# Kernel tuning notes

Measured on AMD Instinct MI355X. Metric: run time of the kernel, lower is better.

## Reference

```python
import jax, jax.numpy as jnp
import numpy as np

H = 16
LN_EPS = 1e-5


def setup_inputs() -> dict:
    key = jax.random.key(0)
    ks = jax.random.split(key, 8)
    B, N, D = 2, 2048, 1024
    s = D ** -0.5
    return {
        "q_s": jax.random.normal(ks[0], (B, N, D), jnp.float32),
        "pos_emb": jax.random.normal(ks[1], (B, N, D), jnp.float32),
        "Wq": jax.random.normal(ks[2], (D, D), jnp.float32) * s,
        "Wk": jax.random.normal(ks[3], (D, D), jnp.float32) * s,
        "Wv": jax.random.normal(ks[4], (D, D), jnp.float32) * s,
        "Wo": jax.random.normal(ks[5], (D, D), jnp.float32) * s,
        "bo": jnp.zeros((D,), jnp.float32),
        "ln_g": jnp.ones((D,), jnp.float32),
        "ln_b": jnp.zeros((D,), jnp.float32),
    }


def _split_heads(t):
    b, n, d = t.shape
    return t.reshape(b, n, H, d // H).transpose(0, 2, 1, 3)  # b h n d


def reference(q_s, pos_emb, Wq, Wk, Wv, Wo, bo, ln_g, ln_b):
    # self-attention: k_s = v_s = q_s
    q = _split_heads(q_s @ Wq)
    k = _split_heads(q_s @ Wk)
    v = _split_heads(q_s @ Wv)
    p = _split_heads(pos_emb)
    scale = q.shape[-1] ** -0.5
    # content-content + content-position attention logits: [b,h,i,j]
    att = (jnp.einsum('bhid,bhjd->bhij', q, k) + jnp.einsum('bhid,bhjd->bhij', q, p)) * scale
    att = jax.nn.softmax(att, axis=-1)
    o = jnp.einsum('bhij,bhjd->bhid', att, v)
    b, h, n, d = o.shape
    o = o.transpose(0, 2, 1, 3).reshape(b, n, h * d)
    o = o @ Wo + bo  # out_layer (dropout rate 0 -> identity)
    x = o + q_s  # residual
    mu = jnp.mean(x, axis=-1, keepdims=True)
    var = jnp.var(x, axis=-1, keepdims=True)
    return (x - mu) * jax.lax.rsqrt(var + LN_EPS) * ln_g + ln_b
```

## Files before the change

kernel.cpp:

```cpp
#include <hip/hip_runtime.h>
#include <hip/hip_bf16.h>
#include <stdint.h>

typedef unsigned short u16;
typedef unsigned int u32;
typedef short s16x8 __attribute__((ext_vector_type(8)));
typedef short s16x4 __attribute__((ext_vector_type(4)));
typedef float f32x4 __attribute__((ext_vector_type(4)));

#define MFMA(a, b, c) __builtin_amdgcn_mfma_f32_16x16x32_bf16((a), (b), (c), 0, 0, 0)

__device__ __forceinline__ float bf2f(u16 h) {
  u32 u = ((u32)h) << 16;
  float f;
  __builtin_memcpy(&f, &u, 4);
  return f;
}

__device__ __forceinline__ u16 f2bf_rte(float f) {
  __hip_bfloat16 h = __float2bfloat16(f);
  u16 u;
  __builtin_memcpy(&u, &h, 2);
  return u;
}

__device__ __forceinline__ void gload16(const u16* g, u16* l) {
  __builtin_amdgcn_global_load_lds((const __attribute__((address_space(1))) u32*)g,
                                   (__attribute__((address_space(3))) u32*)l, 16, 0, 0);
}

__global__ __launch_bounds__(256) void k_prep(const float* __restrict__ q_s,
                                              const float* __restrict__ pos,
                                              const float* __restrict__ W0,
                                              const float* __restrict__ W1,
                                              const float* __restrict__ W2,
                                              const float* __restrict__ W3,
                                              u16* __restrict__ Xbf,
                                              u16* __restrict__ Pp,
                                              u16* __restrict__ WT) {
  __shared__ u16 tile[64][65];
  const int b = blockIdx.x;
  const int t = threadIdx.x;
  if (b < 2048) {
    const int i = b * 256 + t;
    const f32x4* p = (const f32x4*)(q_s + (size_t)i * 8);
    f32x4 a = p[0], bb = p[1];
    s16x8 o;
    for (int k = 0; k < 4; ++k) o[k] = (short)f2bf_rte(a[k]);
    for (int k = 0; k < 4; ++k) o[4 + k] = (short)f2bf_rte(bb[k]);
    *(s16x8*)(Xbf + (size_t)i * 8) = o;
  } else if (b < 3072) {
    const int pb = b - 2048;
    const int bh = pb >> 5, bx = pb & 31;
    const int bq = bh >> 4, h = bh & 15;
    const int n = bx * 64 + (t >> 2);
    const int d0 = (t & 3) * 16;
    const float* src = &pos[((size_t)(bq * 2048 + n)) * 1024 + h * 64 + d0];
    u16* dst = &Pp[((size_t)bh * 2048 + n) * 64 + d0];
    f32x4 a = *(const f32x4*)src;
    f32x4 bq4 = *(const f32x4*)(src + 4);
    f32x4 c = *(const f32x4*)(src + 8);
    f32x4 dq = *(const f32x4*)(src + 12);
    s16x8 o0, o1;
    for (int i = 0; i < 4; ++i) {
      o0[i] = (short)f2bf_rte(a[i]);
      o0[4 + i] = (short)f2bf_rte(bq4[i]);
      o1[i] = (short)f2bf_rte(c[i]);
      o1[4 + i] = (short)f2bf_rte(dq[i]);
    }
    *(s16x8*)dst = o0;
    *(s16x8*)(dst + 8) = o1;
  } else {
    const int wb = b - 3072;
    const int z = wb >> 8, r2 = wb & 255;
    const int bx = r2 & 15, by = r2 >> 4;
    const float* in = (z == 0) ? W0 : (z == 1) ? W1 : (z == 2) ? W2 : W3;
    u16* o = WT + (size_t)z * 1024 * 1024;
    const int tx = t & 63, ty = t >> 6;
    const int r0 = by * 64, c0 = bx * 64;
    for (int rr = 0; rr < 16; ++rr) {
      int row = rr * 4 + ty;
      tile[row][tx] = f2bf_rte(in[(size_t)(r0 + row) * 1024 + c0 + tx]);
    }
    __syncthreads();
    for (int rr = 0; rr < 16; ++rr) {
      int row = rr * 4 + ty;
      o[(size_t)(c0 + row) * 1024 + r0 + tx] = tile[tx][row];
    }
  }
}

__global__ __launch_bounds__(256) void k_transpose_v(const u16* __restrict__ V,
                                                     u16* __restrict__ Vt) {
  __shared__ u16 tile[64][65];
  const int t = threadIdx.x, tx = t & 63, ty = t >> 6;
  const int j0 = blockIdx.x * 64;
  const int bh = blockIdx.y;
  const u16* src = V + (size_t)bh * 2048 * 64;
  u16* dst = Vt + (size_t)bh * 64 * 2048;
  for (int rr = 0; rr < 16; ++rr) {
    int row = rr * 4 + ty;
    tile[row][tx] = src[(size_t)(j0 + row) * 64 + tx];
  }
  __syncthreads();
  for (int rr = 0; rr < 16; ++rr) {
    int d = rr * 4 + ty;
    dst[(size_t)d * 2048 + j0 + tx] = tile[tx][d];
  }
}

__global__ __launch_bounds__(256) void k_qkv_gemm(const u16* __restrict__ X,
                                                  const u16* __restrict__ WT,
                                                  const u16* __restrict__ Pp,
                                                  u16* __restrict__ Qh,
                                                  u16* __restrict__ Kh,
                                                  u16* __restrict__ Vh) {
  __shared__ u16 As[3][4096];
  __shared__ u16 Bs[3][4096];
  const int t = threadIdx.x;
  const int lane = t & 63, wid = t >> 6;
  const int wr = wid >> 1, wc = wid & 1;
  const int g = lane >> 4, lr = lane & 15;
  const int lin = blockIdx.y * 24 + blockIdx.x;
  const int swz = (lin & 7) * 96 + (lin >> 3);
  const int m0 = (swz / 24) * 128, n0 = (swz % 24) * 128;

  const int srcRow = t >> 2;
  const int srcKsw = ((t & 3) * 8) ^ (((t >> 3) & 3) << 3);
  const u16* aSrc = &X[(size_t)(m0 + srcRow) * 1024 + srcKsw];
  const u16* bSrc = &WT[(size_t)(n0 + srcRow) * 1024 + srcKsw];

  const int csw = (g * 8) ^ (((lr >> 1) & 3) << 3);

  f32x4 acc[4][4] = {};

#define QKV_STAGE(buf, k0)                                   \
  {                                                          \
    gload16(aSrc + (k0), &As[buf][wid * 512]);               \
    gload16(aSrc + 65536 + (k0), &As[buf][wid * 512 + 2048]);\
    gload16(bSrc + (k0), &Bs[buf][wid * 512]);               \
    gload16(bSrc + 65536 + (k0), &Bs[buf][wid * 512 + 2048]);\
  }

  QKV_STAGE(0, 0);
  QKV_STAGE(1, 32);
  QKV_STAGE(2, 64);
  for (int k = 0; k < 32; ++k) {
    if (k < 30) {
      asm volatile("s_waitcnt vmcnt(8)" ::: "memory");
    } else if (k == 30) {
      asm volatile("s_waitcnt vmcnt(4)" ::: "memory");
    } else {
      asm volatile("s_waitcnt vmcnt(0)" ::: "memory");
    }
    __builtin_amdgcn_sched_barrier(0);
    __builtin_amdgcn_s_barrier();
    const int cur = k % 3;
    s16x8 a[4], b[4];
#pragma unroll
    for (int mi = 0; mi < 4; ++mi)
      a[mi] = *(const s16x8*)&As[cur][(wr * 64 + mi * 16 + lr) * 32 + csw];
#pragma unroll
    for (int nj = 0; nj < 4; ++nj)
      b[nj] = *(const s16x8*)&Bs[cur][(wc * 64 + nj * 16 + lr) * 32 + csw];
#pragma unroll
    for (int mi = 0; mi < 4; ++mi)
#pragma unroll
      for (int nj = 0; nj < 4; ++nj)
        acc[mi][nj] = MFMA(a[mi], b[nj], acc[mi][nj]);
    __builtin_amdgcn_s_barrier();
    if (k < 29) QKV_STAGE(cur, (k + 3) * 32);
  }
#undef QKV_STAGE

  const float QSCALE = 0.125f * 1.44269504f;
  for (int mi = 0; mi < 4; ++mi) {
    for (int nj = 0; nj < 4; ++nj) {
      const int n_g = n0 + wc * 64 + nj * 16 + lr;
      const int buf = n_g >> 10;
      const int col = n_g & 1023;
      const int h = col >> 6, d = col & 63;
      u16* dst = (buf == 0) ? Qh : ((buf == 1) ? Kh : Vh);
      for (int r = 0; r < 4; ++r) {
        const int row = m0 + wr * 64 + mi * 16 + g * 4 + r;
        const int b = row >> 11, n = row & 2047;
        const size_t off = (size_t)((b * 16 + h) * 2048 + n) * 64 + d;
        float v = acc[mi][nj][r];
        if (buf == 1) v += bf2f(Pp[off]);
        if (buf == 0) v *= QSCALE;
        dst[off] = f2bf_rte(v);
      }
    }
  }
}

__global__ __launch_bounds__(512, 4) void k_attn(const u16* __restrict__ Qh,
                                                 const u16* __restrict__ Kh,
                                                 const u16* __restrict__ Vt,
                                                 u16* __restrict__ Oh) {
  const int t = threadIdx.x, lane = t & 63, wid = t >> 6;
  const int g = lane >> 4, lr = lane & 15;
  const int hid = blockIdx.x;
  const int lid = (hid & 7) * 64 + (hid >> 3);
  const int bh = lid >> 4, itile = lid & 15;
  const int i0 = itile * 128 + wid * 16;

  __shared__ char Ks[4][8192];
  __shared__ char Vs[4][8192];

  const u16* Qp = Qh + (size_t)bh * 2048 * 64;
  const u16* Kp = Kh + (size_t)bh * 2048 * 64;
  const u16* Vp = Vt + (size_t)bh * 64 * 2048;

  s16x8 aq[2];
  aq[0] = *(const s16x8*)&Qp[(size_t)(i0 + lr) * 64 + g * 8];
  aq[1] = *(const s16x8*)&Qp[(size_t)(i0 + lr) * 64 + 32 + g * 8];

  f32x4 oa[4] = {};
  float ms = -1e30f, ls = 0.f;

  const int srow = t >> 3;
  const int sch = (t & 7) * 16;
  const int schS = sch ^ ((srow & 7) << 4);
  const u16* kB = &Kp[(size_t)srow * 64 + (schS >> 1)];
  const u16* vB = &Vp[(size_t)srow * 2048 + (schS >> 1)];

#define ATTN_STAGE(p)                                                \
  {                                                                  \
    gload16(kB + (size_t)(p) * 4096, (u16*)Ks[(p) & 3] + wid * 512); \
    gload16(vB + (size_t)(p) * 64, (u16*)Vs[(p) & 3] + wid * 512);   \
  }

#define ATTN_BODY(BUF)                                                         \
  {                                                                            \
    const char* Kc = Ks[BUF];                                                  \
    const char* Vc = Vs[BUF];                                                  \
    f32x4 s[4] = {};                                                           \
    _Pragma("unroll") for (int jf = 0; jf < 4; ++jf) {                         \
      const int row = jf * 16 + lr;                                            \
      const int bw = (row & 7) << 4;                                           \
      s16x8 bk0 = *(const s16x8*)(Kc + ((row * 128 + g * 16) ^ bw));           \
      s16x8 bk1 = *(const s16x8*)(Kc + ((row * 128 + 64 + g * 16) ^ bw));      \
      s[jf] = MFMA(bk0, aq[0], s[jf]);                                         \
      s[jf] = MFMA(bk1, aq[1], s[jf]);                                         \
    }                                                                          \
    float mj[4];                                                               \
    _Pragma("unroll") for (int jf = 0; jf < 4; ++jf)                           \
        mj[jf] = fmaxf(fmaxf(s[jf][0], s[jf][1]), fmaxf(s[jf][2], s[jf][3]));  \
    float tl = fmaxf(fmaxf(mj[0], mj[1]), fmaxf(mj[2], mj[3]));                \
    if (!__all(tl <= ms + 8.f)) {                                              \
      float tm = fmaxf(tl, __shfl_xor(tl, 16, 64));                            \
      tm = fmaxf(tm, __shfl_xor(tm, 32, 64));                                  \
      float mn = fmaxf(ms, tm);                                                \
      float al = __builtin_amdgcn_exp2f(ms - mn);                              \
      ls *= al;                                                                \
      ms = mn;                                                                 \
      _Pragma("unroll") for (int r = 0; r < 4; ++r) {                          \
        float ab = __shfl(al, g * 4 + r, 64);                                  \
        _Pragma("unroll") for (int df = 0; df < 4; ++df) oa[df][r] *= ab;      \
      }                                                                        \
    }                                                                          \
    float pj[4];                                                               \
    _Pragma("unroll") for (int jf = 0; jf < 4; ++jf) {                         \
      _Pragma("unroll") for (int r = 0; r < 4; ++r)                            \
          s[jf][r] = __builtin_amdgcn_exp2f(s[jf][r] - ms);                    \
      pj[jf] = (s[jf][0] + s[jf][1]) + (s[jf][2] + s[jf][3]);                  \
    }                                                                          \
    ls += (pj[0] + pj[1]) + (pj[2] + pj[3]);                                   \
    u32 pk[4][2];                                                              \
    _Pragma("unroll") for (int jf = 0; jf < 4; ++jf) {                         \
      asm("v_cvt_pk_bf16_f32 %0, %1, %2"                                       \
          : "=v"(pk[jf][0]) : "v"(s[jf][0]), "v"(s[jf][1]));                   \
      asm("v_cvt_pk_bf16_f32 %0, %1, %2"                                       \
          : "=v"(pk[jf][1]) : "v"(s[jf][2]), "v"(s[jf][3]));                   \
    }                                                                          \
    s16x8 pa[2];                                                               \
    _Pragma("unroll") for (int c = 0; c < 2; ++c) {                            \
      u32 w_[4];                                                               \
      _Pragma("unroll") for (int wl = 0; wl < 2; ++wl) {                       \
        u32 A = pk[2 * c][wl], B = pk[2 * c + 1][wl];                          \
        asm("v_permlane32_swap_b32 %0, %1" : "+v"(A), "+v"(B));                \
        asm("v_permlane16_swap_b32 %0, %1" : "+v"(A), "+v"(B));                \
        w_[wl] = A;                                                            \
        w_[2 + wl] = B;                                                        \
      }                                                                        \
      __builtin_memcpy(&pa[c], w_, 16);                                       \
    }                                                                          \
    _Pragma("unroll") for (int df = 0; df < 4; ++df) {                         \
      const int row = df * 16 + lr;                                            \
      const int bw = (row & 7) << 4;                                           \
      s16x8 bv0 = *(const s16x8*)(Vc + ((row * 128 + g * 16) ^ bw));           \
      s16x8 bv1 = *(const s16x8*)(Vc + ((row * 128 + 64 + g * 16) ^ bw));      \
      oa[df] = MFMA(pa[0], bv0, oa[df]);                                       \
      oa[df] = MFMA(pa[1], bv1, oa[df]);                                       \
    }                                                                          \
  }

  ATTN_STAGE(0);
  ATTN_STAGE(1);
  ATTN_STAGE(2);

  for (int tb = 0; tb < 7; ++tb) {
#pragma unroll
    for (int ti = 0; ti < 4; ++ti) {
      const int tt = tb * 4 + ti;
      asm volatile("s_waitcnt vmcnt(4)" ::: "memory");
      __builtin_amdgcn_sched_barrier(0);
      __builtin_amdgcn_s_barrier();
      ATTN_STAGE(tt + 3);
      ATTN_BODY(ti);
    }
  }
  {
    asm volatile("s_waitcnt vmcnt(4)" ::: "memory");
    __builtin_amdgcn_sched_barrier(0);
    __builtin_amdgcn_s_barrier();
    ATTN_STAGE(31);
    ATTN_BODY(0);
  }
  {
    asm volatile("s_waitcnt vmcnt(4)" ::: "memory");
    __builtin_amdgcn_sched_barrier(0);
    __builtin_amdgcn_s_barrier();
    ATTN_BODY(1);
  }
  {
    asm volatile("s_waitcnt vmcnt(2)" ::: "memory");
    __builtin_amdgcn_sched_barrier(0);
    __builtin_amdgcn_s_barrier();
    ATTN_BODY(2);
  }
  {
    asm volatile("s_waitcnt vmcnt(0)" ::: "memory");
    __builtin_amdgcn_sched_barrier(0);
    __builtin_amdgcn_s_barrier();
    ATTN_BODY(3);
  }
#undef ATTN_BODY
#undef ATTN_STAGE

  ls += __shfl_xor(ls, 16, 64);
  ls += __shfl_xor(ls, 32, 64);
  float lb[4];
#pragma unroll
  for (int r = 0; r < 4; ++r) lb[r] = __shfl(ls, g * 4 + r, 64);

  u16* Op = Oh + (size_t)bh * 2048 * 64;
#pragma unroll
  for (int df = 0; df < 4; ++df)
#pragma unroll
    for (int r = 0; r < 4; ++r) {
      const int row0 = i0 + g * 4 + r;
      Op[(size_t)row0 * 64 + df * 16 + lr] = f2bf_rte(oa[df][r] / lb[r]);
    }
}

__global__ __launch_bounds__(256) void k_out_gemm(const u16* __restrict__ Oh,
                                                  const u16* __restrict__ WTo,
                                                  const float* __restrict__ bo,
                                                  const u16* __restrict__ qsb,
                                                  float* __restrict__ X) {
  __shared__ u16 As[3][4096];
  __shared__ u16 Bs[3][4096];
  const int t = threadIdx.x;
  const int lane = t & 63, wid = t >> 6;
  const int wr = wid >> 1, wc = wid & 1;
  const int g = lane >> 4, lr = lane & 15;
  const int lin = blockIdx.y * 8 + blockIdx.x;
  const int swz = (lin & 7) * 32 + (lin >> 3);
  const int m0 = (swz / 8) * 128, n0 = (swz % 8) * 128;

  const int srcRow = t >> 2;
  const int srcKsw = ((t & 3) * 8) ^ (((t >> 3) & 3) << 3);
  const int rg = m0 + srcRow, bb0 = rg >> 11, nn0 = rg & 2047;
  const int rg2 = rg + 64, bb2 = rg2 >> 11, nn2 = rg2 & 2047;
  const u16* bSrc = &WTo[(size_t)(n0 + srcRow) * 1024 + srcKsw];
  const int csw = (g * 8) ^ (((lr >> 1) & 3) << 3);

  f32x4 acc[4][4] = {};

#define OUT_STAGE(buf, k0)                                                        \
  {                                                                               \
    const int h_ = (k0) >> 6, d_ = ((k0) & 63) + srcKsw;                          \
    gload16(&Oh[((size_t)(bb0 * 16 + h_) * 2048 + nn0) * 64 + d_],                \
            &As[buf][wid * 512]);                                                 \
    gload16(&Oh[((size_t)(bb2 * 16 + h_) * 2048 + nn2) * 64 + d_],                \
            &As[buf][wid * 512 + 2048]);                                          \
    gload16(bSrc + (k0), &Bs[buf][wid * 512]);                                    \
    gload16(bSrc + 65536 + (k0), &Bs[buf][wid * 512 + 2048]);                     \
  }

  OUT_STAGE(0, 0);
  OUT_STAGE(1, 32);
  OUT_STAGE(2, 64);
  for (int k = 0; k < 32; ++k) {
    if (k < 30) {
      asm volatile("s_waitcnt vmcnt(8)" ::: "memory");
    } else if (k == 30) {
      asm volatile("s_waitcnt vmcnt(4)" ::: "memory");
    } else {
      asm volatile("s_waitcnt vmcnt(0)" ::: "memory");
    }
    __builtin_amdgcn_sched_barrier(0);
    __builtin_amdgcn_s_barrier();
    const int cur = k % 3;
    s16x8 a[4], b[4];
#pragma unroll
    for (int mi = 0; mi < 4; ++mi)
      a[mi] = *(const s16x8*)&As[cur][(wr * 64 + mi * 16 + lr) * 32 + csw];
#pragma unroll
    for (int nj = 0; nj < 4; ++nj)
      b[nj] = *(const s16x8*)&Bs[cur][(wc * 64 + nj * 16 + lr) * 32 + csw];
#pragma unroll
    for (int mi = 0; mi < 4; ++mi)
#pragma unroll
      for (int nj = 0; nj < 4; ++nj)
        acc[mi][nj] = MFMA(a[mi], b[nj], acc[mi][nj]);
    __builtin_amdgcn_s_barrier();
    if (k < 29) OUT_STAGE(cur, (k + 3) * 32);
  }
#undef OUT_STAGE

  for (int mi = 0; mi < 4; ++mi) {
    for (int nj = 0; nj < 4; ++nj) {
      const int col = n0 + wc * 64 + nj * 16 + lr;
      for (int r = 0; r < 4; ++r) {
        const int row = m0 + wr * 64 + mi * 16 + g * 4 + r;
        float v = acc[mi][nj][r] + bo[col] + bf2f(qsb[(size_t)row * 1024 + col]);
        X[(size_t)row * 1024 + col] = v;
      }
    }
  }
}

__global__ __launch_bounds__(256) void k_ln(const float* __restrict__ X,
                                            const float* __restrict__ gg,
                                            const float* __restrict__ bb,
                                            float* __restrict__ out) {
  const int row = blockIdx.x, t = threadIdx.x;
  const int wid = t >> 6, lane = t & 63;
  const float* xr = X + (size_t)row * 1024;
  f32x4 x = *(const f32x4*)&xr[t * 4];
  float s1 = x[0] + x[1] + x[2] + x[3];
  float s2 = x[0] * x[0] + x[1] * x[1] + x[2] * x[2] + x[3] * x[3];
  for (int off = 32; off > 0; off >>= 1) {
    s1 += __shfl_down(s1, off, 64);
    s2 += __shfl_down(s2, off, 64);
  }
  __shared__ float red[2][4];
  if (lane == 0) { red[0][wid] = s1; red[1][wid] = s2; }
  __syncthreads();
  s1 = red[0][0] + red[0][1] + red[0][2] + red[0][3];
  s2 = red[1][0] + red[1][1] + red[1][2] + red[1][3];
  const float mu = s1 * (1.f / 1024.f);
  const float var = s2 * (1.f / 1024.f) - mu * mu;
  const float rstd = rsqrtf(var + 1e-5f);
  f32x4 gv = *(const f32x4*)&gg[t * 4];
  f32x4 bv = *(const f32x4*)&bb[t * 4];
  f32x4 ov;
  for (int i = 0; i < 4; ++i) ov[i] = (x[i] - mu) * rstd * gv[i] + bv[i];
  *(f32x4*)&out[(size_t)row * 1024 + t * 4] = ov;
}

extern "C" void kernel_launch(void* const* d_in, const int* in_sizes, int n_in,
                              void* d_out, int out_size, void* d_ws, size_t ws_size,
                              hipStream_t stream) {
  (void)in_sizes; (void)n_in; (void)out_size; (void)ws_size;
  const float* q_s = (const float*)d_in[0];
  const float* pos = (const float*)d_in[1];
  const float* Wq = (const float*)d_in[2];
  const float* Wk = (const float*)d_in[3];
  const float* Wv = (const float*)d_in[4];
  const float* Wo = (const float*)d_in[5];
  const float* bo = (const float*)d_in[6];
  const float* lng = (const float*)d_in[7];
  const float* lnb = (const float*)d_in[8];
  float* out = (float*)d_out;

  u16* ws = (u16*)d_ws;
  const size_t MB1 = 1024 * 1024;
  u16* WT  = ws;
  u16* Xbf = ws + 4 * MB1;
  u16* Qh  = Xbf + 4 * MB1;
  u16* Kh  = Qh + 4 * MB1;
  u16* Vh  = Kh + 4 * MB1;
  u16* Vt  = Vh + 4 * MB1;
  u16* Oh  = Vt + 4 * MB1;
  u16* Pp  = Oh;
  float* Xb = (float*)Qh;

  dim3 blk(256);
  k_prep<<<dim3(4096), blk, 0, stream>>>(q_s, pos, Wq, Wk, Wv, Wo, Xbf, Pp, WT);
  k_qkv_gemm<<<dim3(24, 32), blk, 0, stream>>>(Xbf, WT, Pp, Qh, Kh, Vh);
  k_transpose_v<<<dim3(32, 32), blk, 0, stream>>>(Vh, Vt);
  k_attn<<<dim3(512), dim3(512), 0, stream>>>(Qh, Kh, Vt, Oh);
  k_out_gemm<<<dim3(8, 32), blk, 0, stream>>>(Oh, WT + 3 * MB1, bo, Xbf, Xb);
  k_ln<<<4096, blk, 0, stream>>>(Xb, lng, lnb, out);
}
```

Baseline: 143.4 us.

## Use 128-key attention tiles with double buffering and bf16 residual intermediate

The attention kernel now processes 128 keys per iteration instead of 64, with two 16KB K/V buffers in place of four 8KB buffers. The loop waits for all outstanding loads before each tile, so it prefetches only one tile ahead. This halves the number of barriers and softmax rescale checks, at the cost of more registers and a shallower pipeline. Separately, the out-projection GEMM writes its residual sum as bf16 instead of fp32 and the layernorm reads bf16, which cuts intermediate memory traffic but loses precision before normalization.

After: 147.5 us. 2.9% more time.

```diff
diff --git a/kernel.cpp b/kernel.cpp
--- a/kernel.cpp
+++ b/kernel.cpp
@@ -205,8 +205,8 @@
   const int bh = lid >> 4, itile = lid & 15;
   const int i0 = itile * 128 + wid * 16;
 
-  __shared__ char Ks[4][8192];
-  __shared__ char Vs[4][8192];
+  __shared__ char Ks[2][16384];
+  __shared__ char Vs[2][16384];
 
   const u16* Qp = Qh + (size_t)bh * 2048 * 64;
   const u16* Kp = Kh + (size_t)bh * 2048 * 64;
@@ -219,35 +219,44 @@
   f32x4 oa[4] = {};
   float ms = -1e30f, ls = 0.f;
 
-  const int srow = t >> 3;
-  const int sch = (t & 7) * 16;
-  const int schS = sch ^ ((srow & 7) << 4);
-  const u16* kB = &Kp[(size_t)srow * 64 + (schS >> 1)];
-  const u16* vB = &Vp[(size_t)srow * 2048 + (schS >> 1)];
-
-#define ATTN_STAGE(p)                                                \
-  {                                                                  \
-    gload16(kB + (size_t)(p) * 4096, (u16*)Ks[(p) & 3] + wid * 512); \
-    gload16(vB + (size_t)(p) * 64, (u16*)Vs[(p) & 3] + wid * 512);   \
+  const int kRow = t >> 3;
+  const int kCh = (t & 7) * 16;
+  const int kChS = kCh ^ ((kRow & 7) << 4);
+  const u16* kS0 = &Kp[(size_t)kRow * 64 + (kChS >> 1)];
+  const u16* kS1 = &Kp[(size_t)(kRow + 64) * 64 + (kChS >> 1)];
+  const int vRow = t >> 4;
+  const int vCh = (t & 15) * 16;
+  const int vChS = vCh ^ ((vRow & 7) << 4);
+  const u16* vS0 = &Vp[(size_t)vRow * 2048 + (vChS >> 1)];
+  const u16* vS1 = &Vp[(size_t)(vRow + 32) * 2048 + (vChS >> 1)];
+
+#define ATTN_STAGE(p, BUF)                                          \
+  {                                                                 \
+    gload16(kS0 + (size_t)(p) * 8192, (u16*)Ks[BUF] + wid * 512);   \
+    gload16(kS1 + (size_t)(p) * 8192, (u16*)Ks[BUF] + 4096 + wid * 512); \
+    gload16(vS0 + (size_t)(p) * 128, (u16*)Vs[BUF] + wid * 512);    \
+    gload16(vS1 + (size_t)(p) * 128, (u16*)Vs[BUF] + 4096 + wid * 512); \
   }
 
 #define ATTN_BODY(BUF)                                                         \
   {                                                                            \
     const char* Kc = Ks[BUF];                                                  \
     const char* Vc = Vs[BUF];                                                  \
-    f32x4 s[4] = {};                                                           \
-    _Pragma("unroll") for (int jf = 0; jf < 4; ++jf) {                         \
+    f32x4 s[8];                                                                \
+    _Pragma("unroll") for (int jf = 0; jf < 8; ++jf) {                         \
       const int row = jf * 16 + lr;                                            \
       const int bw = (row & 7) << 4;                                           \
       s16x8 bk0 = *(const s16x8*)(Kc + ((row * 128 + g * 16) ^ bw));           \
       s16x8 bk1 = *(const s16x8*)(Kc + ((row * 128 + 64 + g * 16) ^ bw));      \
-      s[jf] = MFMA(bk0, aq[0], s[jf]);                                         \
-      s[jf] = MFMA(bk1, aq[1], s[jf]);                                         \
-    }                                                                          \
-    float mj[4];                                                               \
-    _Pragma("unroll") for (int jf = 0; jf < 4; ++jf)                           \
+      f32x4 z = {};                                                            \
+      z = MFMA(bk0, aq[0], z);                                                 \
+      s[jf] = MFMA(bk1, aq[1], z);                                             \
+    }                                                                          \
+    float mj[8];                                                               \
+    _Pragma("unroll") for (int jf = 0; jf < 8; ++jf)                           \
         mj[jf] = fmaxf(fmaxf(s[jf][0], s[jf][1]), fmaxf(s[jf][2], s[jf][3]));  \
-    float tl = fmaxf(fmaxf(mj[0], mj[1]), fmaxf(mj[2], mj[3]));                \
+    float tl = fmaxf(fmaxf(fmaxf(mj[0], mj[1]), fmaxf(mj[2], mj[3])),          \
+                     fmaxf(fmaxf(mj[4], mj[5]), fmaxf(mj[6], mj[7])));         \
     if (!__all(tl <= ms + 8.f)) {                                              \
       float tm = fmaxf(tl, __shfl_xor(tl, 16, 64));                            \
       tm = fmaxf(tm, __shfl_xor(tm, 32, 64));                                  \
@@ -260,22 +269,23 @@
         _Pragma("unroll") for (int df = 0; df < 4; ++df) oa[df][r] *= ab;      \
       }                                                                        \
     }                                                                          \
-    float pj[4];                                                               \
-    _Pragma("unroll") for (int jf = 0; jf < 4; ++jf) {                         \
+    float pj[8];                                                               \
+    _Pragma("unroll") for (int jf = 0; jf < 8; ++jf) {                         \
       _Pragma("unroll") for (int r = 0; r < 4; ++r)                            \
           s[jf][r] = __builtin_amdgcn_exp2f(s[jf][r] - ms);                    \
       pj[jf] = (s[jf][0] + s[jf][1]) + (s[jf][2] + s[jf][3]);                  \
     }                                                                          \
-    ls += (pj[0] + pj[1]) + (pj[2] + pj[3]);                                   \
-    u32 pk[4][2];                                                              \
-    _Pragma("unroll") for (int jf = 0; jf < 4; ++jf) {                         \
+    ls += ((pj[0] + pj[1]) + (pj[2] + pj[3])) +                                \
+          ((pj[4] + pj[5]) + (pj[6] + pj[7]));                                 \
+    u32 pk[8][2];                                                              \
+    _Pragma("unroll") for (int jf = 0; jf < 8; ++jf) {                         \
       asm("v_cvt_pk_bf16_f32 %0, %1, %2"                                       \
           : "=v"(pk[jf][0]) : "v"(s[jf][0]), "v"(s[jf][1]));                   \
       asm("v_cvt_pk_bf16_f32 %0, %1, %2"                                       \
           : "=v"(pk[jf][1]) : "v"(s[jf][2]), "v"(s[jf][3]));                   \
     }                                                                          \
-    s16x8 pa[2];                                                               \
-    _Pragma("unroll") for (int c = 0; c < 2; ++c) {                            \
+    s16x8 pa[4];                                                               \
+    _Pragma("unroll") for (int c = 0; c < 4; ++c) {                            \
       u32 w_[4];                                                               \
       _Pragma("unroll") for (int wl = 0; wl < 2; ++wl) {                       \
         u32 A = pk[2 * c][wl], B = pk[2 * c + 1][wl];                          \
@@ -284,57 +294,30 @@
         w_[wl] = A;                                                            \
         w_[2 + wl] = B;                                                        \
       }                                                                        \
-      __builtin_memcpy(&pa[c], w_, 16);                                       \
+      __builtin_memcpy(&pa[c], w_, 16);                                        \
     }                                                                          \
     _Pragma("unroll") for (int df = 0; df < 4; ++df) {                         \
       const int row = df * 16 + lr;                                            \
       const int bw = (row & 7) << 4;                                           \
-      s16x8 bv0 = *(const s16x8*)(Vc + ((row * 128 + g * 16) ^ bw));           \
-      s16x8 bv1 = *(const s16x8*)(Vc + ((row * 128 + 64 + g * 16) ^ bw));      \
-      oa[df] = MFMA(pa[0], bv0, oa[df]);                                       \
-      oa[df] = MFMA(pa[1], bv1, oa[df]);                                       \
-    }                                                                          \
-  }
-
-  ATTN_STAGE(0);
-  ATTN_STAGE(1);
-  ATTN_STAGE(2);
-
-  for (int tb = 0; tb < 7; ++tb) {
-#pragma unroll
-    for (int ti = 0; ti < 4; ++ti) {
-      const int tt = tb * 4 + ti;
-      asm volatile("s_waitcnt vmcnt(4)" ::: "memory");
+      _Pragma("unroll") for (int c = 0; c < 4; ++c) {                          \
+        s16x8 bv = *(const s16x8*)(Vc + ((row * 256 + c * 64 + g * 16) ^ bw)); \
+        oa[df] = MFMA(pa[c], bv, oa[df]);                                      \
+      }                                                                        \
+    }                                                                          \
+  }
+
+  ATTN_STAGE(0, 0);
+
+  for (int th = 0; th < 8; ++th) {
+#pragma unroll
+    for (int ti = 0; ti < 2; ++ti) {
+      const int tt = th * 2 + ti;
+      asm volatile("s_waitcnt vmcnt(0)" ::: "memory");
       __builtin_amdgcn_sched_barrier(0);
       __builtin_amdgcn_s_barrier();
-      ATTN_STAGE(tt + 3);
+      if (tt < 15) ATTN_STAGE(tt + 1, ti ^ 1);
       ATTN_BODY(ti);
     }
-  }
-  {
-    asm volatile("s_waitcnt vmcnt(4)" ::: "memory");
-    __builtin_amdgcn_sched_barrier(0);
-    __builtin_amdgcn_s_barrier();
-    ATTN_STAGE(31);
-    ATTN_BODY(0);
-  }
-  {
-    asm volatile("s_waitcnt vmcnt(4)" ::: "memory");
-    __builtin_amdgcn_sched_barrier(0);
-    __builtin_amdgcn_s_barrier();
-    ATTN_BODY(1);
-  }
-  {
-    asm volatile("s_waitcnt vmcnt(2)" ::: "memory");
-    __builtin_amdgcn_sched_barrier(0);
-    __builtin_amdgcn_s_barrier();
-    ATTN_BODY(2);
-  }
-  {
-    asm volatile("s_waitcnt vmcnt(0)" ::: "memory");
-    __builtin_amdgcn_sched_barrier(0);
-    __builtin_amdgcn_s_barrier();
-    ATTN_BODY(3);
   }
 #undef ATTN_BODY
 #undef ATTN_STAGE
@@ -359,7 +342,7 @@
                                                   const u16* __restrict__ WTo,
                                                   const float* __restrict__ bo,
                                                   const u16* __restrict__ qsb,
-                                                  float* __restrict__ X) {
+                                                  u16* __restrict__ X) {
   __shared__ u16 As[3][4096];
   __shared__ u16 Bs[3][4096];
   const int t = threadIdx.x;
@@ -427,22 +410,24 @@
       for (int r = 0; r < 4; ++r) {
         const int row = m0 + wr * 64 + mi * 16 + g * 4 + r;
         float v = acc[mi][nj][r] + bo[col] + bf2f(qsb[(size_t)row * 1024 + col]);
-        X[(size_t)row * 1024 + col] = v;
+        X[(size_t)row * 1024 + col] = f2bf_rte(v);
       }
     }
   }
 }
 
-__global__ __launch_bounds__(256) void k_ln(const float* __restrict__ X,
+__global__ __launch_bounds__(256) void k_ln(const u16* __restrict__ X,
                                             const float* __restrict__ gg,
                                             const float* __restrict__ bb,
                                             float* __restrict__ out) {
   const int row = blockIdx.x, t = threadIdx.x;
   const int wid = t >> 6, lane = t & 63;
-  const float* xr = X + (size_t)row * 1024;
-  f32x4 x = *(const f32x4*)&xr[t * 4];
-  float s1 = x[0] + x[1] + x[2] + x[3];
-  float s2 = x[0] * x[0] + x[1] * x[1] + x[2] * x[2] + x[3] * x[3];
+  const u16* xr = X + (size_t)row * 1024;
+  s16x4 xv = *(const s16x4*)&xr[t * 4];
+  float x[4];
+  for (int i = 0; i < 4; ++i) x[i] = bf2f((u16)xv[i]);
+  float s1 = (x[0] + x[1]) + (x[2] + x[3]);
+  float s2 = (x[0] * x[0] + x[1] * x[1]) + (x[2] * x[2] + x[3] * x[3]);
   for (int off = 32; off > 0; off >>= 1) {
     s1 += __shfl_down(s1, off, 64);
     s2 += __shfl_down(s2, off, 64);
@@ -487,7 +472,7 @@
   u16* Vt  = Vh + 4 * MB1;
   u16* Oh  = Vt + 4 * MB1;
   u16* Pp  = Oh;
-  float* Xb = (float*)Qh;
+  u16* Xb  = Qh;
 
   dim3 blk(256);
   k_prep<<<dim3(4096), blk, 0, stream>>>(q_s, pos, Wq, Wk, Wv, Wo, Xbf, Pp, WT);
```
